# Optimization experiments

Measured on AMD Instinct MI355X. Metric: run time of the kernel, lower is better.

Reference implementation:

```python
import jax, jax.numpy as jnp
import numpy as np

B, N, H, S, C = 32, 64, 128, 100, 16
SIGMA = 0.5  # perturbations.perturbed default noise scale


def setup_inputs() -> dict:
    key = jax.random.key(0)
    ks = jax.random.split(key, 8)
    x = jax.random.normal(ks[0], (B, N, H), jnp.float32)
    a = (jax.random.uniform(ks[1], (B, N, N)) < 0.1).astype(jnp.float32)
    adj = jnp.maximum(a, jnp.swapaxes(a, -1, -2))  # symmetric binary adjacency
    counts = jax.random.randint(ks[2], (B,), N // 2, N + 1)
    mask = jnp.arange(N)[None, :] < counts[:, None]
    sc = 1.0 / np.sqrt(H).astype(np.float32)
    W1 = jax.random.normal(ks[3], (H, H), jnp.float32) * sc
    b1 = jnp.zeros((H,), jnp.float32)
    W2 = jax.random.normal(ks[4], (H, H), jnp.float32) * sc
    b2 = jnp.zeros((H,), jnp.float32)
    cW1 = jax.random.normal(ks[5], (H, H), jnp.float32) * sc
    cb1 = jnp.zeros((H,), jnp.float32)
    cW2 = jax.random.normal(ks[6], (H, C), jnp.float32) * sc
    cb2 = jnp.zeros((C,), jnp.float32)
    noise = jax.random.normal(ks[7], (S * B, N, H), jnp.float32)
    return dict(x=x, adj=adj, mask=mask, W1=W1, b1=b1, W2=W2, b2=b2,
                cW1=cW1, cb1=cb1, cW2=cW2, cb2=cb2, noise=noise, num_samples=S)


def _gcn(x, adj, mask, W, b):
    # DenseGCNConv: set diag to 1, symmetric-normalize, propagate, mask.
    h = x @ W
    n = adj.shape[-1]
    eye = jnp.eye(n, dtype=bool)
    a = jnp.where(eye, 1.0, adj)
    d = jnp.clip(a.sum(-1), 1.0, None) ** -0.5
    a = d[..., :, None] * a * d[..., None, :]
    out = a @ h + b
    return out * mask[..., None].astype(out.dtype)


def _perturbed_clustering(x_all, adj_all, mask_all, cW1, cb1, cW2, cb2):
    BS, n, h = x_all.shape
    # concept MLP + argmax
    logits = jax.nn.relu(x_all @ cW1 + cb1) @ cW2 + cb2
    concepts = jnp.argmax(logits, axis=-1)  # [BS, n]
    same = concepts[:, :, None] == concepts[:, None, :]
    adj_c = jnp.where(same, adj_all, 0.0)
    # connected components via min-label propagation (scipy-order relabel)
    edge = (adj_c > 0) & mask_all[:, :, None] & mask_all[:, None, :]
    labels0 = jnp.where(mask_all, jnp.arange(n, dtype=jnp.int32), n)

    def body(_, labels):
        neigh = jnp.min(jnp.where(edge, labels[:, None, :], n), axis=-1)
        return jnp.minimum(labels, neigh)

    roots = jax.lax.fori_loop(0, n, body, labels0)  # min node idx of component
    present = jnp.zeros((BS, n + 1), jnp.int32).at[
        jnp.arange(BS)[:, None], roots].max(mask_all.astype(jnp.int32))
    rank = jnp.cumsum(present[:, :n], axis=-1)  # 1-based compact id per root
    assignments = jnp.where(
        mask_all,
        jnp.take_along_axis(rank, jnp.minimum(roots, n - 1), axis=-1), 0)
    # scatter-reduce pooling; segment ids flatten (batch, cluster); slot 0 = masked
    seg = (jnp.arange(BS, dtype=jnp.int32)[:, None] * (n + 1) + assignments).reshape(-1)
    x_new = jax.ops.segment_sum(x_all.reshape(BS * n, h), seg,
                                num_segments=BS * (n + 1)).reshape(BS, n + 1, h)[:, 1:]
    row = jax.ops.segment_max(adj_all.reshape(BS * n, n), seg,
                              num_segments=BS * (n + 1)).reshape(BS, n + 1, n)[:, 1:]
    row = jnp.maximum(row, 0.0)  # torch_scatter max includes zero-init
    colsrc = jnp.swapaxes(row, 1, 2).reshape(BS * n, n)
    adj_new = jax.ops.segment_max(colsrc, seg,
                                  num_segments=BS * (n + 1)).reshape(BS, n + 1, n)[:, 1:]
    adj_new = jnp.maximum(jnp.swapaxes(adj_new, 1, 2), 0.0)
    num_clusters = jnp.max(assignments, axis=-1)
    mask_new = jnp.arange(n)[None, :] < num_clusters[:, None]
    return x_new, adj_new, mask_new, assignments


def reference(x, adj, mask, W1, b1, W2, b2, cW1, cb1, cW2, cb2, noise, num_samples):
    # embedding GCN stack
    xe = jax.nn.relu(_gcn(x, adj, mask, W1, b1))
    x_emb = jax.nn.relu(_gcn(xe, adj, mask, W2, b2))
    Bb, n, h = x_emb.shape
    # perturbed replication (sample-major layout, matching final reshape(S, -1, ...))
    adj_all = jnp.tile(adj, (num_samples, 1, 1))
    mask_all = jnp.tile(mask, (num_samples, 1))
    x_all = jnp.tile(x_emb, (num_samples, 1, 1)) + SIGMA * noise
    x_new, adj_new, mask_new, assignments = _perturbed_clustering(
        x_all, adj_all, mask_all, cW1, cb1, cW2, cb2)
    # perturbed expectation for x_new; explicit mean/max in forward for adj/mask
    x_new = x_new.reshape(num_samples, Bb, n, h).mean(axis=0)
    adj_new = adj_new.reshape(num_samples, Bb, n, n).mean(axis=0)
    mask_new = jnp.max(mask_new.reshape(num_samples, Bb, n), axis=0)
    return x_new, adj_new, assignments, x_emb, mask_new
```

## Files before the change

### kernel.cpp

```cpp
#include <hip/hip_runtime.h>
#include <cstdint>

#define B_ 32
#define N_ 64
#define H_ 128
#define S_ 100
#define C_ 16
#define SIGMA_ 0.5f

#define OFF_XNEW 0
#define OFF_ADJN 262144
#define OFF_ASGN 393216
#define OFF_XEMB 598016
#define OFF_MSKN 860160

#define WS_NCL_OFF   0
#define WS_ABITS_OFF 16384
#define WS_MBITS_OFF 32768
#define WS_CONC_OFF  65536
#define WS_CM_OFF    917504
#define WS_ADJB_OFF  2555904
#define WS_XE_OFF    4194304
#define WS_PART_OFF  5242880
#define WS_NEED      57671680ull

__device__ __forceinline__ unsigned short f2bf(float f) {
    unsigned int u = __float_as_uint(f);
    u += 0x7fffu + ((u >> 16) & 1u);
    return (unsigned short)(u >> 16);
}
__device__ __forceinline__ float bf2f(unsigned short h) {
    return __uint_as_float(((unsigned int)h) << 16);
}

__device__ __forceinline__ int read_mask_elem(const void* mp, int idx) {
    const unsigned int* u = (const unsigned int*)mp;
    const unsigned int w0 = u[0], w1 = u[1];
    if (w0 == 1u) {
        if (w1 == 1u) return ((const int*)mp)[idx] != 0;
        return ((const int*)mp)[2 * idx] != 0;
    }
    if (w0 == 0x3f800000u) return ((const float*)mp)[idx] != 0.0f;
    if (w0 == 0u) return ((const double*)mp)[idx] != 0.0;
    return ((const unsigned char*)mp)[idx] != 0;
}

__global__ __launch_bounds__(256) void gcn_stage(
    const float* __restrict__ Xin, const float* __restrict__ adj,
    const void* __restrict__ maskp,
    const float* __restrict__ W, const float* __restrict__ bias,
    float* __restrict__ Xout,
    unsigned long long* __restrict__ abits_ws,
    unsigned long long* __restrict__ mbits_ws, int emit_bits)
{
    const int b = blockIdx.x, cc = blockIdx.y;
    const int t = threadIdx.x;
    const int tj = t & 63, tc = t >> 6;
    __shared__ float Xs[N_][129];
    __shared__ float An[N_][65];
    __shared__ float Hc[N_][20];
    __shared__ float dsh[N_];
    __shared__ unsigned long long mb_sh;

    if (t < 64) {
        const int mv = read_mask_elem(maskp, b * N_ + t);
        const unsigned long long bal = __ballot(mv != 0);
        if (t == 0) { mb_sh = bal; if (emit_bits && cc == 0) mbits_ws[b] = bal; }
    }
    for (int row = (t >> 6); row < N_; row += 4) {
        const int j = t & 63;
        const float v = adj[((size_t)b * N_ + row) * N_ + j];
        const unsigned long long bal = __ballot(v > 0.0f);
        if (emit_bits && cc == 0 && j == 0) abits_ws[b * N_ + row] = bal;
        An[row][j] = (row == j) ? 1.0f : v;
    }
    for (int e = t; e < N_ * H_; e += 256)
        Xs[e >> 7][e & 127] = Xin[(size_t)b * N_ * H_ + e];
    __syncthreads();
    if (t < 64) {
        float s = 0.0f;
        for (int j = 0; j < N_; ++j) s += An[t][j];
        if (s < 1.0f) s = 1.0f;
        dsh[t] = 1.0f / sqrtf(s);
    }
    __syncthreads();
    for (int e = t; e < N_ * N_; e += 256) {
        const int i = e >> 6, j = e & 63;
        An[i][j] *= dsh[i] * dsh[j];
    }
    {
        float a0 = 0, a1 = 0, a2 = 0, a3 = 0;
        const float* wp = W + cc * 16 + tc * 4;
        for (int d = 0; d < H_; ++d) {
            const float xv = Xs[tj][d];
            const float4 w = *(const float4*)(wp + d * H_);
            a0 += xv * w.x; a1 += xv * w.y; a2 += xv * w.z; a3 += xv * w.w;
        }
        float4 o; o.x = a0; o.y = a1; o.z = a2; o.w = a3;
        *(float4*)&Hc[tj][tc * 4] = o;
    }
    __syncthreads();
    {
        float c0 = 0, c1 = 0, c2 = 0, c3 = 0;
        for (int j2 = 0; j2 < N_; ++j2) {
            const float av = An[tj][j2];
            const float4 h = *(const float4*)&Hc[j2][tc * 4];
            c0 += av * h.x; c1 += av * h.y; c2 += av * h.z; c3 += av * h.w;
        }
        const float4 bq = *(const float4*)(bias + cc * 16 + tc * 4);
        const float m = ((mb_sh >> tj) & 1ull) ? 1.0f : 0.0f;
        float4 o;
        o.x = fmaxf(c0 + bq.x, 0.0f) * m; o.y = fmaxf(c1 + bq.y, 0.0f) * m;
        o.z = fmaxf(c2 + bq.z, 0.0f) * m; o.w = fmaxf(c3 + bq.w, 0.0f) * m;
        *(float4*)&Xout[(size_t)b * N_ * H_ + tj * H_ + cc * 16 + tc * 4] = o;
    }
}

__device__ __forceinline__ float rscat16(float* v, int kg) {
#pragma unroll
    for (int i = 0; i < 8; ++i) {
        const float send = (kg & 8) ? v[i] : v[i + 8];
        const float recv = __shfl_xor(send, 8);
        v[i] = ((kg & 8) ? v[i + 8] : v[i]) + recv;
    }
#pragma unroll
    for (int i = 0; i < 4; ++i) {
        const float send = (kg & 4) ? v[i] : v[i + 4];
        const float recv = __shfl_xor(send, 4);
        v[i] = ((kg & 4) ? v[i + 4] : v[i]) + recv;
    }
#pragma unroll
    for (int i = 0; i < 2; ++i) {
        const float send = (kg & 2) ? v[i] : v[i + 2];
        const float recv = __shfl_xor(send, 2);
        v[i] = ((kg & 2) ? v[i + 2] : v[i]) + recv;
    }
    {
        const float send = (kg & 1) ? v[0] : v[1];
        const float recv = __shfl_xor(send, 1);
        v[0] = ((kg & 1) ? v[1] : v[0]) + recv;
    }
    return v[0];
}

__device__ __forceinline__ void argmax16(float bv, int kg, int* dst) {
    int bi = kg;
#pragma unroll
    for (int m = 1; m <= 8; m <<= 1) {
        const float ov = __shfl_xor(bv, m);
        const int   oi = __shfl_xor(bi, m);
        if (ov > bv || (ov == bv && oi < bi)) { bv = ov; bi = oi; }
    }
    if (kg == 0) *dst = bi;
}

__global__ __launch_bounds__(256) void mlp_kernel(
    const float* __restrict__ xemb, const float* __restrict__ noise,
    const float* __restrict__ cW1, const float* __restrict__ cb1,
    const float* __restrict__ cW2, const float* __restrict__ cb2,
    int* __restrict__ conc)
{
    const int sb = blockIdx.x;
    const int b  = sb & (B_ - 1);
    const int t  = threadIdx.x;
    __shared__ float xa[N_ * H_];
    __shared__ float wb[16 * H_];

    {
        const float4* e4 = (const float4*)(xemb + (size_t)b * N_ * H_);
        const float4* n4 = (const float4*)(noise + (size_t)sb * N_ * H_);
        float4* x4 = (float4*)xa;
        for (int idx = t; idx < N_ * 32; idx += 256) {
            const int i = idx >> 5, cc = idx & 31;
            const float4 ev = e4[idx], nv = n4[idx];
            float4 v;
            v.x = ev.x + SIGMA_ * nv.x;  v.y = ev.y + SIGMA_ * nv.y;
            v.z = ev.z + SIGMA_ * nv.z;  v.w = ev.w + SIGMA_ * nv.w;
            x4[i * 32 + (cc ^ (i & 7))] = v;
        }
    }
    __syncthreads();

    const int ng = t >> 4, kg = t & 15;
    float acc[4][8] = {};
    {
        const float4* x4 = (const float4*)xa;
        const int swzb = 4 * (ng & 1);
#pragma unroll 1
        for (int kt = 0; kt < 8; ++kt) {
            if (kt) __syncthreads();
            {
                const float4* wsrc = (const float4*)(cW1 + kt * 16 * H_);
                float4* wd = (float4*)wb;
                wd[t] = wsrc[t];
                wd[t + 256] = wsrc[t + 256];
            }
            __syncthreads();
#pragma unroll
            for (int cc4 = 0; cc4 < 4; ++cc4) {
                const int cc = kt * 4 + cc4;
                float xv[4][4];
#pragma unroll
                for (int r = 0; r < 4; ++r) {
                    const float4 tmp = x4[(4 * ng + r) * 32 + (cc ^ (swzb + r))];
                    xv[r][0] = tmp.x; xv[r][1] = tmp.y; xv[r][2] = tmp.z; xv[r][3] = tmp.w;
                }
#pragma unroll
                for (int dd = 0; dd < 4; ++dd) {
                    const int dl = cc4 * 4 + dd;
                    const float4 wa = *(const float4*)(wb + dl * H_ + 8 * kg);
                    const float4 wc = *(const float4*)(wb + dl * H_ + 8 * kg + 4);
                    const float wf[8] = {wa.x, wa.y, wa.z, wa.w, wc.x, wc.y, wc.z, wc.w};
#pragma unroll
                    for (int j = 0; j < 8; ++j)
#pragma unroll
                        for (int r = 0; r < 4; ++r) acc[r][j] += xv[r][dd] * wf[j];
                }
            }
        }
    }
    {
        const float4 ba = *(const float4*)(cb1 + 8 * kg);
        const float4 bb = *(const float4*)(cb1 + 8 * kg + 4);
        const float bf[8] = {ba.x, ba.y, ba.z, ba.w, bb.x, bb.y, bb.z, bb.w};
        const float cb2v = cb2[kg];
#pragma unroll
        for (int r = 0; r < 4; ++r) {
            float h[8];
#pragma unroll
            for (int j = 0; j < 8; ++j) h[j] = fmaxf(acc[r][j] + bf[j], 0.0f);
            float pl[16] = {};
#pragma unroll
            for (int j = 0; j < 8; ++j) {
                const float4* w2r = (const float4*)(cW2 + (8 * kg + j) * C_);
                const float4 w0 = w2r[0], w1 = w2r[1], w2v = w2r[2], w3 = w2r[3];
                const float wf2[16] = {w0.x, w0.y, w0.z, w0.w, w1.x, w1.y, w1.z, w1.w,
                                       w2v.x, w2v.y, w2v.z, w2v.w, w3.x, w3.y, w3.z, w3.w};
#pragma unroll
                for (int c = 0; c < C_; ++c) pl[c] += h[j] * wf2[c];
            }
            const float l = rscat16(pl, kg) + cb2v;
            argmax16(l, kg, conc + sb * N_ + 4 * ng + r);
        }
    }
}

__global__ __launch_bounds__(256) void cluster_kernel(
    const int* __restrict__ conc,
    const unsigned long long* __restrict__ abits_ws,
    const unsigned long long* __restrict__ mbits_ws,
    unsigned long long* __restrict__ cm_ws,
    unsigned long long* __restrict__ adjbits,
    int* __restrict__ nclArr, float* __restrict__ asgn_out)
{
    const int w = threadIdx.x >> 6, lane = threadIdx.x & 63;
    const int sb = blockIdx.x * 4 + w;
    const int b = sb & (B_ - 1);
    __shared__ int cl[4][N_];
    __shared__ unsigned long long reachL[4][N_];
    __shared__ unsigned long long cmL[4][N_];
    __shared__ unsigned long long roL[4][N_];
    __shared__ unsigned long long abL[4][N_];

    const unsigned long long mb = mbits_ws[b];
    const unsigned long long abv = abits_ws[b * N_ + lane];
    cl[w][lane] = conc[sb * N_ + lane];
    abL[w][lane] = abv;
    cmL[w][lane] = 0ull; roL[w][lane] = 0ull;
    __syncthreads();

    const int masked = (int)((mb >> lane) & 1ull);
    unsigned long long reach = 0ull;
    if (masked) {
        const int ci = cl[w][lane];
        unsigned long long mm = abv & mb, em = 0ull;
        while (mm) {
            const int j = __builtin_ctzll(mm);
            if (cl[w][j] == ci) em |= (1ull << j);
            mm &= mm - 1;
        }
        reach = em | (1ull << lane);
    }
    reachL[w][lane] = reach;
    __syncthreads();
    for (;;) {
        unsigned long long r = reach;
        if (masked) {
            unsigned long long mm = reach & ~(1ull << lane);
            while (mm) {
                const int j = __builtin_ctzll(mm);
                r |= reachL[w][j];
                mm &= mm - 1;
            }
        }
        const int changed = (r != reach);
        __syncthreads();
        reachL[w][lane] = r;
        reach = r;
        if (!__syncthreads_or(changed)) break;
    }
    const int root = masked ? __builtin_ctzll(reach) : 0;
    const unsigned long long present = __ballot(masked && (root == lane));
    const int ncl = __popcll(present);
    const int a_i = masked ? (__popcll(present & ((1ull << root) - 1ull)) + 1) : 0;
    if (masked && root == lane) {
        unsigned long long ro = 0ull, mm = reach;
        while (mm) { const int j = __builtin_ctzll(mm); ro |= abL[w][j]; mm &= mm - 1; }
        cmL[w][a_i - 1] = reach;
        roL[w][a_i - 1] = ro;
    }
    __syncthreads();
    asgn_out[(size_t)sb * N_ + lane] = (float)a_i;
    cm_ws[(size_t)sb * N_ + lane] = cmL[w][lane];
    unsigned long long row = 0ull;
    if (lane < ncl) {
        const unsigned long long ro = roL[w][lane];
        for (int c2 = 0; c2 < ncl; ++c2)
            if (ro & cmL[w][c2]) row |= (1ull << c2);
    }
    adjbits[(size_t)sb * N_ + lane] = row;
    if (lane == 0) nclArr[sb] = ncl;
}

__global__ __launch_bounds__(256) void pool_kernel(
    const float* __restrict__ xemb, const float* __restrict__ noise,
    const unsigned long long* __restrict__ cm_ws,
    unsigned short* __restrict__ part)
{
    const int sb = blockIdx.x;
    const int b  = sb & (B_ - 1);
    const int t  = threadIdx.x;
    const float4* e4 = (const float4*)(xemb + (size_t)b * N_ * H_);
    const float4* n4 = (const float4*)(noise + (size_t)sb * N_ * H_);
    for (int e = t; e < N_ * 32; e += 256) {
        const int c = e >> 5, d4 = e & 31;
        unsigned long long mm = cm_ws[(size_t)sb * N_ + c];
        float4 s = {0.f, 0.f, 0.f, 0.f};
        while (mm) {
            const int j = __builtin_ctzll(mm);
            const float4 ev = e4[j * 32 + d4];
            const float4 nv = n4[j * 32 + d4];
            s.x += ev.x + SIGMA_ * nv.x; s.y += ev.y + SIGMA_ * nv.y;
            s.z += ev.z + SIGMA_ * nv.z; s.w += ev.w + SIGMA_ * nv.w;
            mm &= mm - 1;
        }
        ushort4 o;
        o.x = f2bf(s.x); o.y = f2bf(s.y); o.z = f2bf(s.z); o.w = f2bf(s.w);
        *(ushort4*)&part[(size_t)sb * (N_ * H_) + e * 4] = o;
    }
}

__global__ __launch_bounds__(256) void reduce_kernel(
    const unsigned short* __restrict__ part,
    const unsigned long long* __restrict__ adjbits,
    const int* __restrict__ nclArr, float* __restrict__ out)
{
    const int idx = blockIdx.x * 256 + threadIdx.x;
    if (idx < 65536) {
        const int b = idx >> 11, rem = idx & 2047;
        float4 s = {0.f, 0.f, 0.f, 0.f};
        const unsigned short* p = part + (size_t)b * (N_ * H_) + rem * 4;
#pragma unroll 4
        for (int s_ = 0; s_ < S_; ++s_) {
            const ushort4 v = *(const ushort4*)(p + (size_t)s_ * (B_ * N_ * H_));
            s.x += bf2f(v.x); s.y += bf2f(v.y); s.z += bf2f(v.z); s.w += bf2f(v.w);
        }
        s.x *= 0.01f; s.y *= 0.01f; s.z *= 0.01f; s.w *= 0.01f;
        *(float4*)&out[OFF_XNEW + (size_t)b * (N_ * H_) + rem * 4] = s;
    } else if (idx < 65536 + 131072) {
        const int j = idx - 65536;
        const int b = j >> 12, c1 = (j >> 6) & 63, c2 = j & 63;
        int cnt = 0;
#pragma unroll 4
        for (int s_ = 0; s_ < S_; ++s_)
            cnt += (int)((adjbits[((size_t)s_ * B_ + b) * N_ + c1] >> c2) & 1ull);
        out[OFF_ADJN + j] = (float)cnt * 0.01f;
    } else if (idx < 65536 + 131072 + 2048) {
        const int m = idx - 196608;
        const int b = m >> 6, k = m & 63;
        int mx = 0;
        for (int s_ = 0; s_ < S_; ++s_) {
            const int v = nclArr[s_ * B_ + b];
            mx = v > mx ? v : mx;
        }
        out[OFF_MSKN + m] = (k < mx) ? 1.0f : 0.0f;
    }
}

extern "C" void kernel_launch(void* const* d_in, const int* in_sizes, int n_in,
                              void* d_out, int out_size, void* d_ws, size_t ws_size,
                              hipStream_t stream) {
    (void)in_sizes; (void)n_in; (void)out_size; (void)ws_size;
    const float* x    = (const float*)d_in[0];
    const float* adj  = (const float*)d_in[1];
    const void*  mskp = d_in[2];
    const float* W1   = (const float*)d_in[3];
    const float* b1   = (const float*)d_in[4];
    const float* W2   = (const float*)d_in[5];
    const float* b2   = (const float*)d_in[6];
    const float* cW1  = (const float*)d_in[7];
    const float* cb1  = (const float*)d_in[8];
    const float* cW2  = (const float*)d_in[9];
    const float* cb2  = (const float*)d_in[10];
    const float* noise = (const float*)d_in[11];
    float* out = (float*)d_out;

    int* nclArr = (int*)d_ws;
    unsigned long long* abits_ws = (unsigned long long*)((char*)d_ws + WS_ABITS_OFF);
    unsigned long long* mbits_ws = (unsigned long long*)((char*)d_ws + WS_MBITS_OFF);
    int* conc = (int*)((char*)d_ws + WS_CONC_OFF);
    unsigned long long* cm_ws = (unsigned long long*)((char*)d_ws + WS_CM_OFF);
    unsigned long long* adjbits = (unsigned long long*)((char*)d_ws + WS_ADJB_OFF);
    float* xe_ws = (float*)((char*)d_ws + WS_XE_OFF);
    unsigned short* part = (unsigned short*)((char*)d_ws + WS_PART_OFF);

    float* xemb = out + OFF_XEMB;

    gcn_stage<<<dim3(B_, 8), 256, 0, stream>>>(x, adj, mskp, W1, b1, xe_ws,
                                               abits_ws, mbits_ws, 1);
    gcn_stage<<<dim3(B_, 8), 256, 0, stream>>>(xe_ws, adj, mskp, W2, b2, xemb,
                                               abits_ws, mbits_ws, 0);
    mlp_kernel<<<S_ * B_, 256, 0, stream>>>(xemb, noise, cW1, cb1, cW2, cb2, conc);
    cluster_kernel<<<S_ * B_ / 4, 256, 0, stream>>>(conc, abits_ws, mbits_ws,
                                                    cm_ws, adjbits, nclArr,
                                                    out + OFF_ASGN);
    pool_kernel<<<S_ * B_, 256, 0, stream>>>(xemb, noise, cm_ws, part);
    reduce_kernel<<<(65536 + 131072 + 2048) / 256, 256, 0, stream>>>(
        part, adjbits, nclArr, out);
}
```

Measured before the change: 492.0 us.

## Process two samples per MLP block with 8-row register tiles and prefetched weights

The concept-MLP kernel now handles two perturbed samples per block, giving each 128-thread half its own sample and an 8x8 register accumulator tile instead of 4x8. Each staged cW1 tile in shared memory is therefore reused across twice as many rows. The next weight tile is prefetched into registers while the current one is consumed, and the shared-memory swizzle is changed to match the new row mapping. In exchange, shared memory per block grows to 72KB and register pressure rises, which may lower occupancy.

```diff
diff --git a/kernel.cpp b/kernel.cpp
--- a/kernel.cpp
+++ b/kernel.cpp
@@ -160,49 +160,55 @@
     const float* __restrict__ cW2, const float* __restrict__ cb2,
     int* __restrict__ conc)
 {
-    const int sb = blockIdx.x;
-    const int b  = sb & (B_ - 1);
-    const int t  = threadIdx.x;
-    __shared__ float xa[N_ * H_];
+    const int t = threadIdx.x;
+    const int samp = t >> 7;
+    const int tid  = t & 127;
+    const int kg = tid & 15;
+    const int ng = tid >> 4;
+    const int sb = blockIdx.x * 2 + samp;
+
+    __shared__ float xa[2 * N_ * H_];
     __shared__ float wb[16 * H_];
 
     {
-        const float4* e4 = (const float4*)(xemb + (size_t)b * N_ * H_);
-        const float4* n4 = (const float4*)(noise + (size_t)sb * N_ * H_);
         float4* x4 = (float4*)xa;
-        for (int idx = t; idx < N_ * 32; idx += 256) {
-            const int i = idx >> 5, cc = idx & 31;
-            const float4 ev = e4[idx], nv = n4[idx];
+        for (int idx = t; idx < 2 * N_ * 32; idx += 256) {
+            const int s = idx >> 11, r2 = idx & 2047;
+            const int i = r2 >> 5, cc = r2 & 31;
+            const int sbl = blockIdx.x * 2 + s;
+            const int bl  = sbl & (B_ - 1);
+            const float4 ev = ((const float4*)(xemb + (size_t)bl * N_ * H_))[r2];
+            const float4 nv = ((const float4*)(noise + (size_t)sbl * N_ * H_))[r2];
             float4 v;
             v.x = ev.x + SIGMA_ * nv.x;  v.y = ev.y + SIGMA_ * nv.y;
             v.z = ev.z + SIGMA_ * nv.z;  v.w = ev.w + SIGMA_ * nv.w;
-            x4[i * 32 + (cc ^ (i & 7))] = v;
-        }
-    }
-    __syncthreads();
-
-    const int ng = t >> 4, kg = t & 15;
-    float acc[4][8] = {};
-    {
-        const float4* x4 = (const float4*)xa;
-        const int swzb = 4 * (ng & 1);
+            x4[s * 2048 + i * 32 + (cc ^ ((i & 7) ^ (i >> 3)))] = v;
+        }
+    }
+
+    float acc[8][8] = {};
+    {
+        const float4* x4s = (const float4*)(xa + samp * N_ * H_);
+        const float4* wsrc = (const float4*)cW1;
+        float4 p0 = wsrc[t], p1 = wsrc[t + 256];
+        const int gg = ng;
 #pragma unroll 1
         for (int kt = 0; kt < 8; ++kt) {
-            if (kt) __syncthreads();
-            {
-                const float4* wsrc = (const float4*)(cW1 + kt * 16 * H_);
-                float4* wd = (float4*)wb;
-                wd[t] = wsrc[t];
-                wd[t + 256] = wsrc[t + 256];
+            __syncthreads();
+            ((float4*)wb)[t] = p0;
+            ((float4*)wb)[t + 256] = p1;
+            __syncthreads();
+            if (kt < 7) {
+                p0 = wsrc[(kt + 1) * 512 + t];
+                p1 = wsrc[(kt + 1) * 512 + t + 256];
             }
-            __syncthreads();
 #pragma unroll
             for (int cc4 = 0; cc4 < 4; ++cc4) {
                 const int cc = kt * 4 + cc4;
-                float xv[4][4];
-#pragma unroll
-                for (int r = 0; r < 4; ++r) {
-                    const float4 tmp = x4[(4 * ng + r) * 32 + (cc ^ (swzb + r))];
+                float xv[8][4];
+#pragma unroll
+                for (int r = 0; r < 8; ++r) {
+                    const float4 tmp = x4s[(8 * ng + r) * 32 + (cc ^ (r ^ gg))];
                     xv[r][0] = tmp.x; xv[r][1] = tmp.y; xv[r][2] = tmp.z; xv[r][3] = tmp.w;
                 }
 #pragma unroll
@@ -214,7 +220,7 @@
 #pragma unroll
                     for (int j = 0; j < 8; ++j)
 #pragma unroll
-                        for (int r = 0; r < 4; ++r) acc[r][j] += xv[r][dd] * wf[j];
+                        for (int r = 0; r < 8; ++r) acc[r][j] += xv[r][dd] * wf[j];
                 }
             }
         }
@@ -225,7 +231,7 @@
         const float bf[8] = {ba.x, ba.y, ba.z, ba.w, bb.x, bb.y, bb.z, bb.w};
         const float cb2v = cb2[kg];
 #pragma unroll
-        for (int r = 0; r < 4; ++r) {
+        for (int r = 0; r < 8; ++r) {
             float h[8];
 #pragma unroll
             for (int j = 0; j < 8; ++j) h[j] = fmaxf(acc[r][j] + bf[j], 0.0f);
@@ -240,7 +246,7 @@
                 for (int c = 0; c < C_; ++c) pl[c] += h[j] * wf2[c];
             }
             const float l = rscat16(pl, kg) + cb2v;
-            argmax16(l, kg, conc + sb * N_ + 4 * ng + r);
+            argmax16(l, kg, conc + sb * N_ + 8 * ng + r);
         }
     }
 }
@@ -420,7 +426,7 @@
                                                abits_ws, mbits_ws, 1);
     gcn_stage<<<dim3(B_, 8), 256, 0, stream>>>(xe_ws, adj, mskp, W2, b2, xemb,
                                                abits_ws, mbits_ws, 0);
-    mlp_kernel<<<S_ * B_, 256, 0, stream>>>(xemb, noise, cW1, cb1, cW2, cb2, conc);
+    mlp_kernel<<<S_ * B_ / 2, 256, 0, stream>>>(xemb, noise, cW1, cb1, cW2, cb2, conc);
     cluster_kernel<<<S_ * B_ / 4, 256, 0, stream>>>(conc, abits_ws, mbits_ws,
                                                     cm_ws, adjbits, nclArr,
                                                     out + OFF_ASGN);
```

Measured after the change: 622.0 us. +26.4%, slower.
